# Kernel optimization log

Measured on AMD Instinct MI355X. Metric: run time of the kernel, lower is better.

Reference implementation:

```python
import jax, jax.numpy as jnp
from jax import lax
import numpy as np

# Dims matching init_kwargs
V = 32000      # vocab
D = 768        # d_model
L = 4          # n_layers
N = 16         # state_size
K = 4          # conv kernel
I = 2 * D      # intermediate = expand * d_model = 1536
DT = (D + 15) // 16  # time_step_rank = 48
BATCH, SEQ = 4, 2048
EPS = 1e-5


def setup_inputs() -> dict:
    key = jax.random.key(0)
    ks = jax.random.split(key, 12)
    s = 0.02
    A_init = jnp.broadcast_to(jnp.arange(1, N + 1, dtype=jnp.float32), (L, I, N))
    return {
        "input_ids": jax.random.randint(ks[0], (BATCH, SEQ), 0, V, dtype=jnp.int32),
        "embed": jax.random.normal(ks[1], (V, D), jnp.float32) * s,        # tied lm_head
        "norm_w": jnp.ones((L, D), jnp.float32),
        "in_proj_w": jax.random.normal(ks[2], (L, 2 * I, D), jnp.float32) * s,
        "conv_w": jax.random.normal(ks[3], (L, I, K), jnp.float32) * s,
        "conv_b": jnp.zeros((L, I), jnp.float32),
        "x_proj_w": jax.random.normal(ks[4], (L, DT + 2 * N, I), jnp.float32) * s,
        "dt_proj_w": jax.random.normal(ks[5], (L, I, DT), jnp.float32) * s,
        "dt_proj_b": jax.random.normal(ks[6], (L, I), jnp.float32) * s,
        "A_log": jnp.log(A_init),
        "D_param": jnp.ones((L, I), jnp.float32),
        "out_proj_w": jax.random.normal(ks[7], (L, D, I), jnp.float32) * s,
        "norm_f_w": jnp.ones((D,), jnp.float32),
    }


def rmsnorm(x, w):
    return x * lax.rsqrt(jnp.mean(x * x, axis=-1, keepdims=True) + EPS) * w


def mamba_mixer(x, in_w, cw, cb, xp_w, dtp_w, dtp_b, a_log, d_par, out_w):
    # x: [B, S, D]
    proj = jnp.einsum('bsd,ed->bse', x, in_w)            # [B, S, 2I]
    u, gate = jnp.split(proj, 2, axis=-1)                # each [B, S, I]
    # causal depthwise conv1d (HF pads K-1 then truncates to S == left pad)
    uc = u.transpose(0, 2, 1)                            # [B, I, S]
    conv = lax.conv_general_dilated(
        uc, cw[:, None, :], window_strides=(1,), padding=[(K - 1, 0)],
        feature_group_count=I, dimension_numbers=('NCH', 'OIH', 'NCH'))
    ut = jax.nn.silu(conv + cb[None, :, None]).transpose(0, 2, 1)  # [B, S, I]
    # SSM parameters
    xdbl = jnp.einsum('bsi,ei->bse', ut, xp_w)           # [B, S, DT+2N]
    dt_r = xdbl[..., :DT]
    Bm = xdbl[..., DT:DT + N]                            # [B, S, N]
    Cm = xdbl[..., DT + N:]                              # [B, S, N]
    dt = jax.nn.softplus(jnp.einsum('bsr,ir->bsi', dt_r, dtp_w) + dtp_b)  # [B, S, I]
    A = -jnp.exp(a_log)                                  # [I, N]

    def step(h, ins):
        dt_t, B_t, C_t, u_t = ins                        # [B,I],[B,N],[B,N],[B,I]
        dA = jnp.exp(dt_t[..., None] * A)                # [B, I, N]
        h = dA * h + (dt_t[..., None] * B_t[:, None, :]) * u_t[..., None]
        y = jnp.einsum('bin,bn->bi', h, C_t)
        return h, y

    h0 = jnp.zeros((x.shape[0], I, N), x.dtype)
    xs = (dt.transpose(1, 0, 2), Bm.transpose(1, 0, 2),
          Cm.transpose(1, 0, 2), ut.transpose(1, 0, 2))
    _, ys = lax.scan(step, h0, xs)                       # [S, B, I]
    y = ys.transpose(1, 0, 2) + ut * d_par               # skip D term
    y = y * jax.nn.silu(gate)
    return jnp.einsum('bsi,di->bsd', y, out_w)           # [B, S, D]


def reference(input_ids, embed, norm_w, in_proj_w, conv_w, conv_b, x_proj_w,
              dt_proj_w, dt_proj_b, A_log, D_param, out_proj_w, norm_f_w):
    h = embed[input_ids]                                 # [B, S, D]
    for l in range(L):
        h = h + mamba_mixer(rmsnorm(h, norm_w[l]), in_proj_w[l], conv_w[l],
                            conv_b[l], x_proj_w[l], dt_proj_w[l], dt_proj_b[l],
                            A_log[l], D_param[l], out_proj_w[l])
    h = rmsnorm(h, norm_f_w)
    # module returns logits[:, -1]; compute only last-token logits (tied lm_head)
    return h[:, -1] @ embed.T                            # [B, V]
```

## Files before the change

kernel.cpp:

```cpp
#include <hip/hip_runtime.h>
#include <hip/hip_bf16.h>

#define Vv 32000
#define Dm 768
#define Lm 4
#define Nst 16
#define Kc 4
#define Im 1536
#define DTr 48
#define Bt 4
#define Sq 2048
#define TOK (Bt*Sq)
#define EPSf 1e-5f
#define NC 64
#define CL 32
#define QROWS (Bt*NC*16)
#define LOG2E 1.4426950408889634f
#define LN2f  0.6931471805599453f

using bf16 = __hip_bfloat16;
typedef __bf16 bf16x8 __attribute__((ext_vector_type(8)));
typedef float f32x4 __attribute__((ext_vector_type(4)));

__device__ __forceinline__ float b2f(bf16 x){ return __bfloat162float(x); }
__device__ __forceinline__ bf16 f2b(float x){ return __float2bfloat16(x); }
__device__ __forceinline__ float us2f(ushort u){ unsigned x = (unsigned)u << 16; return __builtin_bit_cast(float, x); }

__device__ __forceinline__ float ex2(float x){
#if __has_builtin(__builtin_amdgcn_exp2f)
  return __builtin_amdgcn_exp2f(x);
#else
  float r; asm("v_exp_f32 %0, %1" : "=v"(r) : "v"(x)); return r;
#endif
}
__device__ __forceinline__ float vlog2(float x){
#if __has_builtin(__builtin_amdgcn_logf)
  return __builtin_amdgcn_logf(x);
#else
  float r; asm("v_log_f32 %0, %1" : "=v"(r) : "v"(x)); return r;
#endif
}
__device__ __forceinline__ float frcp(float x){
#if __has_builtin(__builtin_amdgcn_rcpf)
  return __builtin_amdgcn_rcpf(x);
#else
  float r; asm("v_rcp_f32 %0, %1" : "=v"(r) : "v"(x)); return r;
#endif
}

#define GLDS(gp, lp) __builtin_amdgcn_global_load_lds( \
    (const __attribute__((address_space(1))) void*)(gp), \
    (__attribute__((address_space(3))) void*)(lp), 16, 0, 0)

__global__ __launch_bounds__(256) void k_cvt(const float* __restrict__ src,
                                             bf16* __restrict__ dst, int n){
  int i = (blockIdx.x*256 + threadIdx.x)*4;
  if (i >= n) return;
  float4 v = *(const float4*)(src + i);
  bf16* o = dst + i;
  o[0]=f2b(v.x); o[1]=f2b(v.y); o[2]=f2b(v.z); o[3]=f2b(v.w);
}

__global__ __launch_bounds__(256) void k_cvt_xpw(const float* __restrict__ src,
                                                 bf16* __restrict__ dst){
  int idx = blockIdx.x*256 + threadIdx.x;
  int l = idx / (128*Im); int rem = idx - l*128*Im;
  int r = rem / Im;       int c = rem - r*Im;
  dst[idx] = (r < 80) ? f2b(src[((size_t)l*80 + r)*Im + c]) : f2b(0.f);
}

__global__ __launch_bounds__(256) void k_cvt_dtw(const float* __restrict__ src,
                                                 bf16* __restrict__ dst){
  int idx = blockIdx.x*256 + threadIdx.x;
  int l = idx / (Im*64); int rem = idx - l*Im*64;
  int r = rem / 64;      int c = rem - r*64;
  dst[idx] = (c < 48) ? f2b(src[((size_t)l*Im + r)*48 + c]) : f2b(0.f);
}

__global__ __launch_bounds__(256) void k_embed(const int* __restrict__ ids,
                                               const float* __restrict__ emb,
                                               float* __restrict__ h){
  int t = blockIdx.x;
  const float4* e = (const float4*)(emb + (size_t)ids[t]*Dm);
  float4* o = (float4*)(h + (size_t)t*Dm);
  if (threadIdx.x < Dm/4) o[threadIdx.x] = e[threadIdx.x];
}

__global__ __launch_bounds__(256) void k_rmsnorm(const float* __restrict__ h,
                                                 const float* __restrict__ w,
                                                 bf16* __restrict__ xb){
  int t = blockIdx.x;
  const float* x = h + (size_t)t*Dm;
  float v[3]; float ss = 0.f;
  #pragma unroll
  for (int j=0;j<3;j++){ v[j] = x[threadIdx.x + j*256]; ss += v[j]*v[j]; }
  #pragma unroll
  for (int off=32; off; off>>=1) ss += __shfl_xor(ss, off);
  __shared__ float sred[4];
  int wave = threadIdx.x>>6, lane = threadIdx.x&63;
  if (lane==0) sred[wave]=ss;
  __syncthreads();
  float tot = sred[0]+sred[1]+sred[2]+sred[3];
  float scale = rsqrtf(tot*(1.f/Dm) + EPSf);
  bf16* o = xb + (size_t)t*Dm;
  #pragma unroll
  for (int j=0;j<3;j++){ int d = threadIdx.x + j*256; o[d] = f2b(v[j]*scale*w[d]); }
}

__global__ __launch_bounds__(256) void k_rms_last(const float* __restrict__ h,
                                                  const float* __restrict__ w,
                                                  float* __restrict__ xf){
  int b = blockIdx.x;
  const float* x = h + ((size_t)b*Sq + (Sq-1))*Dm;
  float v[3]; float ss = 0.f;
  #pragma unroll
  for (int j=0;j<3;j++){ v[j] = x[threadIdx.x + j*256]; ss += v[j]*v[j]; }
  #pragma unroll
  for (int off=32; off; off>>=1) ss += __shfl_xor(ss, off);
  __shared__ float sred[4];
  int wave = threadIdx.x>>6, lane = threadIdx.x&63;
  if (lane==0) sred[wave]=ss;
  __syncthreads();
  float tot = sred[0]+sred[1]+sred[2]+sred[3];
  float scale = rsqrtf(tot*(1.f/Dm) + EPSf);
  float* o = xf + (size_t)b*Dm;
  #pragma unroll
  for (int j=0;j<3;j++){ int d = threadIdx.x + j*256; o[d] = v[j]*scale*w[d]; }
}

template<int MODE>
__global__ __launch_bounds__(256) void k_gemm(const bf16* __restrict__ A,
                                              const bf16* __restrict__ Bw,
                                              void* __restrict__ Cout,
                                              const float* __restrict__ bias,
                                              int M, int N, int K,
                                              int lda, int ldb, int ldc){
  __shared__ __align__(16) ushort Ash[128*32];
  __shared__ __align__(16) ushort Bsh[128*32];
  int tid = threadIdx.x;
  int bm = blockIdx.y, bn = blockIdx.x;
  int wave = tid >> 6, lane = tid & 63;
  int wrow = wave >> 1, wcol = wave & 1;
  int quad = lane >> 4, lq = lane & 15;

  f32x4 acc[4][4];
  #pragma unroll
  for (int a=0;a<4;a++)
    #pragma unroll
    for (int b=0;b<4;b++) acc[a][b] = (f32x4){0.f,0.f,0.f,0.f};

  const ushort* Ag = (const ushort*)A;
  const ushort* Bg = (const ushort*)Bw;

  for (int k0 = 0; k0 < K; k0 += 32) {
    __syncthreads();
    #pragma unroll
    for (int c = tid; c < 512; c += 256) {
      int row = c >> 2, col = (c & 3) * 8;
      GLDS(&Ag[(size_t)(bm*128 + row)*lda + k0 + col], &Ash[c*8]);
      GLDS(&Bg[(size_t)(bn*128 + row)*ldb + k0 + col], &Bsh[c*8]);
    }
    __syncthreads();
    bf16x8 af[4], bfr[4];
    #pragma unroll
    for (int a=0;a<4;a++){
      int m = wrow*64 + a*16 + lq;
      af[a] = __builtin_bit_cast(bf16x8, *(const uint4*)&Ash[m*32 + quad*8]);
    }
    #pragma unroll
    for (int b=0;b<4;b++){
      int n = wcol*64 + b*16 + lq;
      bfr[b] = __builtin_bit_cast(bf16x8, *(const uint4*)&Bsh[n*32 + quad*8]);
    }
    #pragma unroll
    for (int a=0;a<4;a++)
      #pragma unroll
      for (int b=0;b<4;b++)
        acc[a][b] = __builtin_amdgcn_mfma_f32_16x16x32_bf16(af[a], bfr[b], acc[a][b], 0, 0, 0);
  }
  #pragma unroll
  for (int a=0;a<4;a++)
    #pragma unroll
    for (int b=0;b<4;b++)
      #pragma unroll
      for (int r=0;r<4;r++){
        int row = bm*128 + wrow*64 + a*16 + quad*4 + r;
        int col = bn*128 + wcol*64 + b*16 + lq;
        size_t idx = (size_t)row*ldc + col;
        if (MODE == 0) ((bf16*)Cout)[idx] = f2b(acc[a][b][r]);
        else if (MODE == 1) ((float*)Cout)[idx] += acc[a][b][r];
        else {
          float v = acc[a][b][r] + bias[col];
          float sp;
          if (v > 20.f) sp = v;
          else { float e = ex2(v*LOG2E); sp = vlog2(1.f + e)*LN2f; }
          ((float*)Cout)[idx] = sp;
        }
      }
}

#define SA256(qm,k0s,bf_) { GLDS(Ag + sA[qm][0] + (k0s), lds + (bf_)*32768 + lA[qm][0]); \
                            GLDS(Ag + sA[qm][1] + (k0s), lds + (bf_)*32768 + lA[qm][1]); }
#define SB256(qn,k0s,bf_) { GLDS(Bg + sB[qn][0] + (k0s), lds + 65536 + (bf_)*32768 + lB[qn][0]); \
                            GLDS(Bg + sB[qn][1] + (k0s), lds + 65536 + (bf_)*32768 + lB[qn][1]); }
#define RD_A(qm_) do{ _Pragma("unroll") for(int m2=0;m2<4;m2++){ \
    int r = wm*128 + ((qm_)*4+m2)*16 + lq; \
    _Pragma("unroll") for(int kh=0;kh<2;kh++) \
      bA[m2][kh] = *(const uint4*)(Ab + (r<<7) + ((kh*64 + quad*16) ^ ((r&7)<<4))); } }while(0)
#define RD_B(qn_) do{ _Pragma("unroll") for(int n2=0;n2<2;n2++){ \
    int r = wn*64 + ((qn_)*2+n2)*16 + lq; \
    _Pragma("unroll") for(int kh=0;kh<2;kh++) \
      bB[qn_][n2][kh] = *(const uint4*)(Bb + (r<<7) + ((kh*64 + quad*16) ^ ((r&7)<<4))); } }while(0)
#define MMA256(qm_,qn_) do{ \
  __builtin_amdgcn_s_barrier(); \
  __builtin_amdgcn_sched_barrier(0); \
  __builtin_amdgcn_s_setprio(1); \
  _Pragma("unroll") for(int m2=0;m2<4;m2++) \
    _Pragma("unroll") for(int n2=0;n2<2;n2++) \
      _Pragma("unroll") for(int kh=0;kh<2;kh++) \
        acc[(qm_)*4+m2][(qn_)*2+n2] = __builtin_amdgcn_mfma_f32_16x16x32_bf16( \
          __builtin_bit_cast(bf16x8, bA[m2][kh]), __builtin_bit_cast(bf16x8, bB[qn_][n2][kh]), \
          acc[(qm_)*4+m2][(qn_)*2+n2], 0, 0, 0); \
  __builtin_amdgcn_s_setprio(0); \
  __builtin_amdgcn_s_barrier(); \
  __builtin_amdgcn_sched_barrier(0); \
}while(0)
#define VMW4 asm volatile("s_waitcnt vmcnt(4)":::"memory")

template<int MODE>
__global__ __launch_bounds__(512, 2) void k_gemm256(const bf16* __restrict__ A,
                                                    const bf16* __restrict__ Bw,
                                                    void* __restrict__ Cout,
                                                    int M, int N, int K,
                                                    int lda, int ldb, int ldc){
  __shared__ __align__(16) char lds[131072];
  int tid = threadIdx.x;
  int wave = tid >> 6, lane = tid & 63;
  int wm = wave >> 2, wn = wave & 3;
  int quad = lane >> 4, lq = lane & 15;
  int nx = gridDim.x;
  int nwg = nx * gridDim.y;
  int lin = blockIdx.y * nx + blockIdx.x;
  if ((nwg & 7) == 0){
    int cpx = nwg >> 3;
    lin = (lin & 7)*cpx + (lin >> 3);
  }
  int bm = lin / nx, bn = lin - bm*nx;
  const ushort* Ag = (const ushort*)A;
  const ushort* Bg = (const ushort*)Bw;

  size_t sA[2][2]; int lA[2][2];
  size_t sB[2][2]; int lB[2][2];
  #pragma unroll
  for (int qm=0; qm<2; qm++)
    #pragma unroll
    for (int d=0; d<2; d++){
      int r = d*128 + qm*64 + (tid>>3);
      int cb = ((tid&7)<<4) ^ ((r&7)<<4);
      sA[qm][d] = (size_t)(bm*256 + r)*lda + (cb>>1);
      lA[qm][d] = ((d*128 + qm*64)<<7) + tid*16;
    }
  #pragma unroll
  for (int qn=0; qn<2; qn++)
    #pragma unroll
    for (int d=0; d<2; d++){
      int g = 2*d + (wave>>2);
      int jj = tid & 255;
      int r = g*64 + qn*32 + (jj>>3);
      int cb = ((jj&7)<<4) ^ ((r&7)<<4);
      sB[qn][d] = (size_t)(bn*256 + r)*ldb + (cb>>1);
      lB[qn][d] = ((g*64 + qn*32)<<7) + jj*16;
    }

  f32x4 acc[8][4];
  #pragma unroll
  for (int a=0;a<8;a++)
    #pragma unroll
    for (int b=0;b<4;b++) acc[a][b] = (f32x4){0.f,0.f,0.f,0.f};

  SA256(0, 0, 0); SB256(0, 0, 0); SB256(1, 0, 0); SA256(1, 0, 0);
  VMW4;
  __builtin_amdgcn_s_barrier();
  __builtin_amdgcn_sched_barrier(0);

  uint4 bA[4][2], bB[2][2][2];
  int NT = K >> 6;
  for (int t = 0; t < NT-1; t++){
    int buf = t & 1, bufn = buf ^ 1;
    int k0n = (t+1) << 6;
    const char* Ab = lds + buf*32768;
    const char* Bb = lds + 65536 + buf*32768;
    RD_A(0); RD_B(0); SA256(0,k0n,bufn); VMW4; MMA256(0,0);
    RD_B(1);          SB256(0,k0n,bufn); VMW4; MMA256(0,1);
    RD_A(1);          SB256(1,k0n,bufn);       MMA256(1,0);
                      SA256(1,k0n,bufn); VMW4; MMA256(1,1);
  }
  {
    int buf = (NT-1) & 1;
    const char* Ab = lds + buf*32768;
    const char* Bb = lds + 65536 + buf*32768;
    RD_A(0); RD_B(0); asm volatile("s_waitcnt vmcnt(2)":::"memory"); MMA256(0,0);
    RD_B(1);          asm volatile("s_waitcnt vmcnt(0)":::"memory"); MMA256(0,1);
    RD_A(1);                                                          MMA256(1,0);
                                                                      MMA256(1,1);
  }

  #pragma unroll
  for (int mr=0; mr<8; mr++)
    #pragma unroll
    for (int nr=0; nr<4; nr++)
      #pragma unroll
      for (int rr=0; rr<4; rr++){
        int row = bm*256 + wm*128 + mr*16 + quad*4 + rr;
        int col = bn*256 + wn*64 + nr*16 + lq;
        size_t idx = (size_t)row*ldc + col;
        if (MODE == 0) ((bf16*)Cout)[idx] = f2b(acc[mr][nr][rr]);
        else ((float*)Cout)[idx] += acc[mr][nr][rr];
      }
}

__global__ __launch_bounds__(256) void k_conv(const bf16* __restrict__ proj,
                                              const float* __restrict__ cw,
                                              const float* __restrict__ cb,
                                              bf16* __restrict__ ut){
  int t = blockIdx.y;
  int i = blockIdx.x*256 + threadIdx.x;
  int s = t & (Sq-1);
  float acc = cb[i];
  #pragma unroll
  for (int k=0;k<Kc;k++){
    int sk = s + k - 3;
    if (sk >= 0) acc += b2f(proj[(size_t)(t+k-3)*(2*Im) + i]) * cw[i*Kc+k];
  }
  float sig = frcp(1.f + ex2(-acc*LOG2E));
  ut[(size_t)t*Im + i] = f2b(acc*sig);
}


__global__ __launch_bounds__(256) void k_scan1(const float* __restrict__ dt,
                                               const bf16* __restrict__ ut,
                                               const bf16* __restrict__ xdbl,
                                               const float* __restrict__ alog,
                                               bf16* __restrict__ Qb,
                                               float* __restrict__ S){
  __shared__ float s_b[CL][16];
  int tid = threadIdx.x;
  int i = blockIdx.x*256 + tid;
  int b = blockIdx.y, c = blockIdx.z;
  size_t tok0 = (size_t)b*Sq + c*CL;
  {
    int row = tid >> 1, part = tid & 1;
    if (row < CL){
      uint4 v = *(const uint4*)((const ushort*)xdbl + (tok0+row)*128 + 48 + part*8);
      const ushort* u = (const ushort*)&v;
      #pragma unroll
      for (int j=0;j<8;j++) s_b[row][part*8+j] = us2f(u[j]);
    }
  }
  float kn[16];
  {
    const float4* ap = (const float4*)(alog + (size_t)i*16);
    #pragma unroll
    for (int q=0;q<4;q++){
      float4 a4 = ap[q];
      kn[q*4+0] = -__expf(a4.x)*LOG2E; kn[q*4+1] = -__expf(a4.y)*LOG2E;
      kn[q*4+2] = -__expf(a4.z)*LOG2E; kn[q*4+3] = -__expf(a4.w)*LOG2E;
    }
  }
  bool fastp = true;
  #pragma unroll
  for (int n=1;n<16;n++)
    fastp = fastp && (fabsf(kn[n] - (float)(n+1)*kn[0]) <= 1e-4f*fabsf(kn[n]));
  __syncthreads();
  float h[16];
  #pragma unroll
  for (int n=0;n<16;n++) h[n]=0.f;
  float sum = 0.f;
  float dtn = dt[tok0*Im + i];
  ushort un = ((const ushort*)ut)[tok0*Im + i];
  if (fastp){
    float k0 = kn[0];
    for (int t = 0; t < CL; t++){
      float dtv = dtn; float uv = us2f(un);
      if (t+1 < CL){
        dtn = dt[(tok0+t+1)*Im + i];
        un  = ((const ushort*)ut)[(tok0+t+1)*Im + i];
      }
      sum += dtv;
      float cdu = dtv*uv;
      const f32x4* brow = (const f32x4*)&s_b[t][0];
      f32x4 B0=brow[0], B1=brow[1], B2=brow[2], B3=brow[3];
      float Bv[16] = {B0[0],B0[1],B0[2],B0[3],B1[0],B1[1],B1[2],B1[3],
                      B2[0],B2[1],B2[2],B2[3],B3[0],B3[1],B3[2],B3[3]};
      float p1 = ex2(k0*dtv);
      float p2=p1*p1, p3=p2*p1, p4=p2*p2;
      float p5=p4*p1, p6=p4*p2, p7=p4*p3, p8=p4*p4;
      float d[16] = {p1,p2,p3,p4,p5,p6,p7,p8,
                     p8*p1,p8*p2,p8*p3,p8*p4,p8*p5,p8*p6,p8*p7,p8*p8};
      #pragma unroll
      for (int n=0;n<16;n++)
        h[n] = d[n]*h[n] + cdu*Bv[n];
    }
  } else {
    for (int t = 0; t < CL; t++){
      float dtv = dtn; float uv = us2f(un);
      if (t+1 < CL){
        dtn = dt[(tok0+t+1)*Im + i];
        un  = ((const ushort*)ut)[(tok0+t+1)*Im + i];
      }
      sum += dtv;
      float cdu = dtv*uv;
      const f32x4* brow = (const f32x4*)&s_b[t][0];
      f32x4 B0=brow[0], B1=brow[1], B2=brow[2], B3=brow[3];
      float Bv[16] = {B0[0],B0[1],B0[2],B0[3],B1[0],B1[1],B1[2],B1[3],
                      B2[0],B2[1],B2[2],B2[3],B3[0],B3[1],B3[2],B3[3]};
      #pragma unroll
      for (int n=0;n<16;n++)
        h[n] = ex2(kn[n]*dtv)*h[n] + cdu*Bv[n];
    }
  }
  int rq = (b*NC + c)*16;
  S[(size_t)(b*NC + c)*Im + i] = sum;
  #pragma unroll
  for (int n=0;n<16;n++)
    Qb[(size_t)(rq+n)*2*Im + i] = f2b(h[n]);
}

__global__ __launch_bounds__(256) void k_scan2(const bf16* __restrict__ Qb,
                                               const float* __restrict__ S,
                                               const float* __restrict__ alog,
                                               bf16* __restrict__ Hinb){
  int idx = blockIdx.x*256 + threadIdx.x;
  int i = idx % Im; int bn = idx / Im;
  int n = bn & 15, b = bn >> 4;
  float kn = -__expf(alog[(size_t)i*16 + n])*LOG2E;
  float h = 0.f;
  for (int c = 0; c < NC; c++){
    size_t r = (size_t)((b*NC + c)*16 + n);
    Hinb[(QROWS + r)*2*Im + i] = f2b(h);
    float P = ex2(kn * S[(size_t)(b*NC + c)*Im + i]);
    h = P*h + b2f(Qb[r*2*Im + i]);
  }
}

__global__ __launch_bounds__(256) void k_scan3(const float* __restrict__ dt,
                                               const bf16* __restrict__ ut,
                                               const bf16* __restrict__ xdbl,
                                               const bf16* __restrict__ proj,
                                               const float* __restrict__ alog,
                                               const float* __restrict__ dpar,
                                               const bf16* __restrict__ Hinb,
                                               bf16* __restrict__ y){
  __shared__ float s_bc[CL][32];
  int tid = threadIdx.x;
  int i = blockIdx.x*256 + tid;
  int b = blockIdx.y, c = blockIdx.z;
  size_t tok0 = (size_t)b*Sq + c*CL;
  {
    int row = tid >> 1, part = tid & 1;
    if (row < CL){
      const ushort* src = (const ushort*)xdbl + (tok0+row)*128 + 48 + part*16;
      uint4 v0 = *(const uint4*)src;
      uint4 v1 = *(const uint4*)(src + 8);
      const ushort* u0 = (const ushort*)&v0;
      const ushort* u1 = (const ushort*)&v1;
      #pragma unroll
      for (int j=0;j<8;j++){
        s_bc[row][part*16 + j]     = us2f(u0[j]);
        s_bc[row][part*16 + 8 + j] = us2f(u1[j]);
      }
    }
  }
  float kn[16];
  {
    const float4* ap = (const float4*)(alog + (size_t)i*16);
    #pragma unroll
    for (int q=0;q<4;q++){
      float4 a4 = ap[q];
      kn[q*4+0] = -__expf(a4.x)*LOG2E; kn[q*4+1] = -__expf(a4.y)*LOG2E;
      kn[q*4+2] = -__expf(a4.z)*LOG2E; kn[q*4+3] = -__expf(a4.w)*LOG2E;
    }
  }
  bool fastp = true;
  #pragma unroll
  for (int n=1;n<16;n++)
    fastp = fastp && (fabsf(kn[n] - (float)(n+1)*kn[0]) <= 1e-4f*fabsf(kn[n]));
  float Dp = dpar[i];
  float h[16];
  {
    int rq = QROWS + (b*NC + c)*16;
    #pragma unroll
    for (int n=0;n<16;n++)
      h[n] = b2f(Hinb[(size_t)(rq+n)*2*Im + i]);
  }
  __syncthreads();
  float dtn = dt[tok0*Im + i];
  ushort un = ((const ushort*)ut)[tok0*Im + i];
  ushort gn = ((const ushort*)proj)[tok0*2*Im + Im + i];
  if (fastp){
    float k0 = kn[0];
    for (int t = 0; t < CL; t++){
      float dtv = dtn; float uv = us2f(un); float g = us2f(gn);
      if (t+1 < CL){
        dtn = dt[(tok0+t+1)*Im + i];
        un  = ((const ushort*)ut)[(tok0+t+1)*Im + i];
        gn  = ((const ushort*)proj)[(tok0+t+1)*2*Im + Im + i];
      }
      float cdu = dtv*uv;
      const f32x4* brow = (const f32x4*)&s_bc[t][0];
      f32x4 B0=brow[0], B1=brow[1], B2=brow[2], B3=brow[3];
      f32x4 C0=brow[4], C1=brow[5], C2=brow[6], C3=brow[7];
      float Bv[16] = {B0[0],B0[1],B0[2],B0[3],B1[0],B1[1],B1[2],B1[3],
                      B2[0],B2[1],B2[2],B2[3],B3[0],B3[1],B3[2],B3[3]};
      float Cv[16] = {C0[0],C0[1],C0[2],C0[3],C1[0],C1[1],C1[2],C1[3],
                      C2[0],C2[1],C2[2],C2[3],C3[0],C3[1],C3[2],C3[3]};
      float p1 = ex2(k0*dtv);
      float p2=p1*p1, p3=p2*p1, p4=p2*p2;
      float p5=p4*p1, p6=p4*p2, p7=p4*p3, p8=p4*p4;
      float d[16] = {p1,p2,p3,p4,p5,p6,p7,p8,
                     p8*p1,p8*p2,p8*p3,p8*p4,p8*p5,p8*p6,p8*p7,p8*p8};
      float yv = 0.f;
      #pragma unroll
      for (int n=0;n<16;n++){
        h[n] = d[n]*h[n] + cdu*Bv[n];
        yv += h[n]*Cv[n];
      }
      float sig = frcp(1.f + ex2(-g*LOG2E));
      float outv = (yv + uv*Dp) * (g*sig);
      y[(tok0+t)*Im + i] = f2b(outv);
    }
  } else {
    for (int t = 0; t < CL; t++){
      float dtv = dtn; float uv = us2f(un); float g = us2f(gn);
      if (t+1 < CL){
        dtn = dt[(tok0+t+1)*Im + i];
        un  = ((const ushort*)ut)[(tok0+t+1)*Im + i];
        gn  = ((const ushort*)proj)[(tok0+t+1)*2*Im + Im + i];
      }
      float cdu = dtv*uv;
      const f32x4* brow = (const f32x4*)&s_bc[t][0];
      f32x4 B0=brow[0], B1=brow[1], B2=brow[2], B3=brow[3];
      f32x4 C0=brow[4], C1=brow[5], C2=brow[6], C3=brow[7];
      float Bv[16] = {B0[0],B0[1],B0[2],B0[3],B1[0],B1[1],B1[2],B1[3],
                      B2[0],B2[1],B2[2],B2[3],B3[0],B3[1],B3[2],B3[3]};
      float Cv[16] = {C0[0],C0[1],C0[2],C0[3],C1[0],C1[1],C1[2],C1[3],
                      C2[0],C2[1],C2[2],C2[3],C3[0],C3[1],C3[2],C3[3]};
      float yv = 0.f;
      #pragma unroll
      for (int n=0;n<16;n++){
        h[n] = ex2(kn[n]*dtv)*h[n] + cdu*Bv[n];
        yv += h[n]*Cv[n];
      }
      float sig = frcp(1.f + ex2(-g*LOG2E));
      float outv = (yv + uv*Dp) * (g*sig);
      y[(tok0+t)*Im + i] = f2b(outv);
    }
  }
}

__global__ __launch_bounds__(256) void k_logits(const float* __restrict__ xf,
                                                const float* __restrict__ emb,
                                                float* __restrict__ out){
  __shared__ __align__(16) float xs[Bt*Dm];
  for (int j = threadIdx.x; j < Bt*Dm; j += 256) xs[j] = xf[j];
  __syncthreads();
  int wave = threadIdx.x>>6, lane = threadIdx.x&63;
  int v = blockIdx.x*4 + wave;
  const float4* e4 = (const float4*)(emb + (size_t)v*Dm);
  float a0=0.f,a1=0.f,a2=0.f,a3=0.f;
  for (int j = lane; j < Dm/4; j += 64){
    float4 ev = e4[j];
    float4 x0 = *(const float4*)&xs[j*4];
    float4 x1 = *(const float4*)&xs[Dm + j*4];
    float4 x2 = *(const float4*)&xs[2*Dm + j*4];
    float4 x3 = *(const float4*)&xs[3*Dm + j*4];
    a0 += ev.x*x0.x + ev.y*x0.y + ev.z*x0.z + ev.w*x0.w;
    a1 += ev.x*x1.x + ev.y*x1.y + ev.z*x1.z + ev.w*x1.w;
    a2 += ev.x*x2.x + ev.y*x2.y + ev.z*x2.z + ev.w*x2.w;
    a3 += ev.x*x3.x + ev.y*x3.y + ev.z*x3.z + ev.w*x3.w;
  }
  #pragma unroll
  for (int off=32; off; off>>=1){
    a0+=__shfl_xor(a0,off); a1+=__shfl_xor(a1,off);
    a2+=__shfl_xor(a2,off); a3+=__shfl_xor(a3,off);
  }
  if (lane==0){
    out[v]        = a0;
    out[Vv+v]     = a1;
    out[2*Vv+v]   = a2;
    out[3*Vv+v]   = a3;
  }
}

extern "C" void kernel_launch(void* const* d_in, const int* in_sizes, int n_in,
                              void* d_out, int out_size, void* d_ws, size_t ws_size,
                              hipStream_t stream){
  const int*   ids   = (const int*)d_in[0];
  const float* emb   = (const float*)d_in[1];
  const float* normw = (const float*)d_in[2];
  const float* inw   = (const float*)d_in[3];
  const float* cw    = (const float*)d_in[4];
  const float* cb    = (const float*)d_in[5];
  const float* xpw   = (const float*)d_in[6];
  const float* dtw   = (const float*)d_in[7];
  const float* dtb   = (const float*)d_in[8];
  const float* alog  = (const float*)d_in[9];
  const float* dpar  = (const float*)d_in[10];
  const float* outw  = (const float*)d_in[11];
  const float* normf = (const float*)d_in[12];
  float* out = (float*)d_out;

  char* p = (char*)d_ws;
  float* h    = (float*)p;  p += (size_t)TOK*Dm*4;
  bf16*  xb   = (bf16*)p;   p += (size_t)TOK*Dm*2;
  bf16*  proj = (bf16*)p;   p += (size_t)TOK*2*Im*2;
  bf16*  utb  = (bf16*)p;   p += (size_t)TOK*Im*2;
  bf16*  xdbl = (bf16*)p;   p += (size_t)TOK*128*2;
  float* dtf  = (float*)p;  p += (size_t)TOK*Im*4;
  bf16*  yb   = (bf16*)p;   p += (size_t)TOK*Im*2;
  float* xf   = (float*)p;  p += (size_t)Bt*Dm*4;
  bf16*  inwb = (bf16*)p;   p += (size_t)Lm*2*Im*Dm*2;
  bf16*  outwb= (bf16*)p;   p += (size_t)Lm*Dm*Im*2;
  bf16*  xpwb = (bf16*)p;   p += (size_t)Lm*128*Im*2;
  bf16*  dtwb = (bf16*)p;   p += (size_t)Lm*Im*64*2;
  float* S = (float*)xb;

  { int n = Lm*2*Im*Dm; k_cvt<<<n/1024, 256, 0, stream>>>(inw, inwb, n); }
  { int n = Lm*Dm*Im;   k_cvt<<<n/1024, 256, 0, stream>>>(outw, outwb, n); }
  k_cvt_xpw<<<(Lm*128*Im)/256, 256, 0, stream>>>(xpw, xpwb);
  k_cvt_dtw<<<(Lm*Im*64)/256, 256, 0, stream>>>(dtw, dtwb);

  k_embed<<<TOK, 256, 0, stream>>>(ids, emb, h);

  for (int l = 0; l < Lm; l++){
    k_rmsnorm<<<TOK, 256, 0, stream>>>(h, normw + l*Dm, xb);
    k_gemm256<0><<<dim3((2*Im)/256, TOK/256), 512, 0, stream>>>(
        xb, inwb + (size_t)l*2*Im*Dm, proj, TOK, 2*Im, Dm, Dm, Dm, 2*Im);
    k_conv<<<dim3(Im/256, TOK), 256, 0, stream>>>(
        proj, cw + (size_t)l*Im*Kc, cb + (size_t)l*Im, utb);
    k_gemm<0><<<dim3(1, TOK/128), 256, 0, stream>>>(
        utb, xpwb + (size_t)l*128*Im, xdbl, nullptr, TOK, 128, Im, Im, Im, 128);
    k_gemm<3><<<dim3(Im/128, TOK/128), 256, 0, stream>>>(
        xdbl, dtwb + (size_t)l*Im*64, dtf, dtb + (size_t)l*Im, TOK, Im, 64, 128, 64, Im);
    k_scan1<<<dim3(Im/256, Bt, NC), 256, 0, stream>>>(
        dtf, utb, xdbl, alog + (size_t)l*Im*Nst, proj, S);
    k_scan2<<<(Bt*Nst*Im)/256, 256, 0, stream>>>(
        proj, S, alog + (size_t)l*Im*Nst, proj);
    k_scan3<<<dim3(Im/256, Bt, NC), 256, 0, stream>>>(
        dtf, utb, xdbl, proj, alog + (size_t)l*Im*Nst, dpar + (size_t)l*Im, proj, yb);
    k_gemm<1><<<dim3(Dm/128, TOK/128), 256, 0, stream>>>(
        yb, outwb + (size_t)l*Dm*Im, h, nullptr, TOK, Dm, Im, Im, Im, Dm);
  }

  k_rms_last<<<Bt, 256, 0, stream>>>(h, normf, xf);
  k_logits<<<Vv/4, 256, 0, stream>>>(xf, emb, out);
}
```

Before: 1.410 ms.

## Store dt in bf16, deepen scan prefetch, use 256-tile GEMM for out_proj

```diff
diff --git a/kernel.cpp b/kernel.cpp
--- a/kernel.cpp
+++ b/kernel.cpp
@@ -194,7 +194,7 @@
           float sp;
           if (v > 20.f) sp = v;
           else { float e = ex2(v*LOG2E); sp = vlog2(1.f + e)*LN2f; }
-          ((float*)Cout)[idx] = sp;
+          ((bf16*)Cout)[idx] = f2b(sp);
         }
       }
 }
@@ -337,7 +337,7 @@
 }
 
 
-__global__ __launch_bounds__(256) void k_scan1(const float* __restrict__ dt,
+__global__ __launch_bounds__(256) void k_scan1(const bf16* __restrict__ dt,
                                                const bf16* __restrict__ ut,
                                                const bf16* __restrict__ xdbl,
                                                const float* __restrict__ alog,
@@ -376,15 +376,18 @@
   #pragma unroll
   for (int n=0;n<16;n++) h[n]=0.f;
   float sum = 0.f;
-  float dtn = dt[tok0*Im + i];
-  ushort un = ((const ushort*)ut)[tok0*Im + i];
+  const ushort* dtp = (const ushort*)dt + tok0*Im + i;
+  const ushort* utp = (const ushort*)ut + tok0*Im + i;
+  ushort dA = dtp[0], uA = utp[0];
+  ushort dB = dtp[Im], uB = utp[Im];
   if (fastp){
     float k0 = kn[0];
     for (int t = 0; t < CL; t++){
-      float dtv = dtn; float uv = us2f(un);
-      if (t+1 < CL){
-        dtn = dt[(tok0+t+1)*Im + i];
-        un  = ((const ushort*)ut)[(tok0+t+1)*Im + i];
+      float dtv = us2f(dA); float uv = us2f(uA);
+      dA = dB; uA = uB;
+      if (t+2 < CL){
+        dB = dtp[(size_t)(t+2)*Im];
+        uB = utp[(size_t)(t+2)*Im];
       }
       sum += dtv;
       float cdu = dtv*uv;
@@ -403,10 +406,11 @@
     }
   } else {
     for (int t = 0; t < CL; t++){
-      float dtv = dtn; float uv = us2f(un);
-      if (t+1 < CL){
-        dtn = dt[(tok0+t+1)*Im + i];
-        un  = ((const ushort*)ut)[(tok0+t+1)*Im + i];
+      float dtv = us2f(dA); float uv = us2f(uA);
+      dA = dB; uA = uB;
+      if (t+2 < CL){
+        dB = dtp[(size_t)(t+2)*Im];
+        uB = utp[(size_t)(t+2)*Im];
       }
       sum += dtv;
       float cdu = dtv*uv;
@@ -443,7 +447,7 @@
   }
 }
 
-__global__ __launch_bounds__(256) void k_scan3(const float* __restrict__ dt,
+__global__ __launch_bounds__(256) void k_scan3(const bf16* __restrict__ dt,
                                                const bf16* __restrict__ ut,
                                                const bf16* __restrict__ xdbl,
                                                const bf16* __restrict__ proj,
@@ -494,17 +498,20 @@
       h[n] = b2f(Hinb[(size_t)(rq+n)*2*Im + i]);
   }
   __syncthreads();
-  float dtn = dt[tok0*Im + i];
-  ushort un = ((const ushort*)ut)[tok0*Im + i];
-  ushort gn = ((const ushort*)proj)[tok0*2*Im + Im + i];
+  const ushort* dtp = (const ushort*)dt + tok0*Im + i;
+  const ushort* utp = (const ushort*)ut + tok0*Im + i;
+  const ushort* gp  = (const ushort*)proj + tok0*2*Im + Im + i;
+  ushort dA = dtp[0], uA = utp[0], gA = gp[0];
+  ushort dB = dtp[Im], uB = utp[Im], gB = gp[2*Im];
   if (fastp){
     float k0 = kn[0];
     for (int t = 0; t < CL; t++){
-      float dtv = dtn; float uv = us2f(un); float g = us2f(gn);
-      if (t+1 < CL){
-        dtn = dt[(tok0+t+1)*Im + i];
-        un  = ((const ushort*)ut)[(tok0+t+1)*Im + i];
-        gn  = ((const ushort*)proj)[(tok0+t+1)*2*Im + Im + i];
+      float dtv = us2f(dA); float uv = us2f(uA); float g = us2f(gA);
+      dA = dB; uA = uB; gA = gB;
+      if (t+2 < CL){
+        dB = dtp[(size_t)(t+2)*Im];
+        uB = utp[(size_t)(t+2)*Im];
+        gB = gp[(size_t)(t+2)*2*Im];
       }
       float cdu = dtv*uv;
       const f32x4* brow = (const f32x4*)&s_bc[t][0];
@@ -531,11 +538,12 @@
     }
   } else {
     for (int t = 0; t < CL; t++){
-      float dtv = dtn; float uv = us2f(un); float g = us2f(gn);
-      if (t+1 < CL){
-        dtn = dt[(tok0+t+1)*Im + i];
-        un  = ((const ushort*)ut)[(tok0+t+1)*Im + i];
-        gn  = ((const ushort*)proj)[(tok0+t+1)*2*Im + Im + i];
+      float dtv = us2f(dA); float uv = us2f(uA); float g = us2f(gA);
+      dA = dB; uA = uB; gA = gB;
+      if (t+2 < CL){
+        dB = dtp[(size_t)(t+2)*Im];
+        uB = utp[(size_t)(t+2)*Im];
+        gB = gp[(size_t)(t+2)*2*Im];
       }
       float cdu = dtv*uv;
       const f32x4* brow = (const f32x4*)&s_bc[t][0];
@@ -616,7 +624,7 @@
   bf16*  proj = (bf16*)p;   p += (size_t)TOK*2*Im*2;
   bf16*  utb  = (bf16*)p;   p += (size_t)TOK*Im*2;
   bf16*  xdbl = (bf16*)p;   p += (size_t)TOK*128*2;
-  float* dtf  = (float*)p;  p += (size_t)TOK*Im*4;
+  bf16*  dtq  = (bf16*)p;   p += (size_t)TOK*Im*2;
   bf16*  yb   = (bf16*)p;   p += (size_t)TOK*Im*2;
   float* xf   = (float*)p;  p += (size_t)Bt*Dm*4;
   bf16*  inwb = (bf16*)p;   p += (size_t)Lm*2*Im*Dm*2;
@@ -641,15 +649,15 @@
     k_gemm<0><<<dim3(1, TOK/128), 256, 0, stream>>>(
         utb, xpwb + (size_t)l*128*Im, xdbl, nullptr, TOK, 128, Im, Im, Im, 128);
     k_gemm<3><<<dim3(Im/128, TOK/128), 256, 0, stream>>>(
-        xdbl, dtwb + (size_t)l*Im*64, dtf, dtb + (size_t)l*Im, TOK, Im, 64, 128, 64, Im);
+        xdbl, dtwb + (size_t)l*Im*64, dtq, dtb + (size_t)l*Im, TOK, Im, 64, 128, 64, Im);
     k_scan1<<<dim3(Im/256, Bt, NC), 256, 0, stream>>>(
-        dtf, utb, xdbl, alog + (size_t)l*Im*Nst, proj, S);
+        dtq, utb, xdbl, alog + (size_t)l*Im*Nst, proj, S);
     k_scan2<<<(Bt*Nst*Im)/256, 256, 0, stream>>>(
         proj, S, alog + (size_t)l*Im*Nst, proj);
     k_scan3<<<dim3(Im/256, Bt, NC), 256, 0, stream>>>(
-        dtf, utb, xdbl, proj, alog + (size_t)l*Im*Nst, dpar + (size_t)l*Im, proj, yb);
-    k_gemm<1><<<dim3(Dm/128, TOK/128), 256, 0, stream>>>(
-        yb, outwb + (size_t)l*Dm*Im, h, nullptr, TOK, Dm, Im, Im, Im, Dm);
+        dtq, utb, xdbl, proj, alog + (size_t)l*Im*Nst, dpar + (size_t)l*Im, proj, yb);
+    k_gemm256<1><<<dim3(Dm/256, TOK/256), 512, 0, stream>>>(
+        yb, outwb + (size_t)l*Dm*Im, h, TOK, Dm, Im, Im, Im, Dm);
   }
 
   k_rms_last<<<Bt, 256, 0, stream>>>(h, normf, xf);
```

Measured after the change: 1.520 ms. 7.8% more time.
